# Kernel tuning notes

Measured on AMD Instinct MI355X. Metric: run time of the kernel, lower is better.

## Reference

```python
import jax, jax.numpy as jnp
import numpy as np

B, T, K = 16, 512, 128  # batch, seq_len, num_state


def setup_inputs() -> dict:
    key = jax.random.key(0)
    k1, k2, k3 = jax.random.split(key, 3)
    transition = jax.random.normal(k1, (K, K), dtype=jnp.float32)
    emission = jax.random.normal(k2, (B, T, K), dtype=jnp.float32)
    seq_lens = jax.random.randint(k3, (B,), 1, T + 1)  # lengths in [1, T]
    return {"transition": transition, "emission": emission, "seq_lens": seq_lens}


def reference(transition, emission, seq_lens):
    # potential_normalization='none' -> identity normalize().
    # combine_potentials: log phi[b, t, y_{t-1}, y_t] = trans[y_{t-1}, y_t] + emis[b, t, y_t]
    log_pot = transition[None, None, :, :] + emission[:, :, None, :]  # [B,T,K,K]

    alpha0 = emission[:, 0, :]  # [B,K]

    def step(alpha_prev, pot_t):  # alpha_prev: [B,K], pot_t: [B,K,K]
        alpha_t = jax.nn.logsumexp(alpha_prev[:, :, None] + pot_t, axis=1)
        return alpha_t, alpha_t

    # scan over time steps 1..T-1 (time-major potentials)
    _, alphas_rest = jax.lax.scan(step, alpha0, jnp.swapaxes(log_pot[:, 1:], 0, 1))
    alpha = jnp.concatenate(
        [alpha0[:, None, :], jnp.swapaxes(alphas_rest, 0, 1)], axis=1
    )  # [B,T,K]

    # gather alpha at position seq_lens - 1 per batch element
    last = jnp.take_along_axis(alpha, (seq_lens - 1)[:, None, None], axis=1)[:, 0, :]
    log_Z = jax.nn.logsumexp(last, axis=-1)  # [B]
    return alpha, log_Z
```

## Files before the change

kernel.cpp:

```cpp
#include <hip/hip_runtime.h>
#include <math.h>

#define KDIM 128
#define TLEN 512
#define BATCH 16
#define CH_L 16
#define NCH 32
#define NMAT 31

typedef _Float16 half8 __attribute__((ext_vector_type(8)));
typedef _Float16 half4 __attribute__((ext_vector_type(4)));
typedef _Float16 half2t __attribute__((ext_vector_type(2)));
typedef float floatx4 __attribute__((ext_vector_type(4)));

#if defined(__has_builtin)
#if __has_builtin(__builtin_amdgcn_fdot2)
#define HAVE_FDOT2 1
#endif
#endif

static __device__ __forceinline__ float dot2f(half2t a, half2t b, float c) {
#ifdef HAVE_FDOT2
    return __builtin_amdgcn_fdot2(a, b, c, false);
#else
    return fmaf((float)a[0], (float)b[0], fmaf((float)a[1], (float)b[1], c));
#endif
}

static __device__ __forceinline__ float dot8(const half8 v, const float4 w, float acc) {
    const uint4 r = __builtin_bit_cast(uint4, v);
    acc = dot2f(__builtin_bit_cast(half2t, w.x), __builtin_bit_cast(half2t, r.x), acc);
    acc = dot2f(__builtin_bit_cast(half2t, w.y), __builtin_bit_cast(half2t, r.y), acc);
    acc = dot2f(__builtin_bit_cast(half2t, w.z), __builtin_bit_cast(half2t, r.z), acc);
    acc = dot2f(__builtin_bit_cast(half2t, w.w), __builtin_bit_cast(half2t, r.w), acc);
    return acc;
}

static __device__ __forceinline__ void gload_lds16(const _Float16* g, _Float16* l) {
    __builtin_amdgcn_global_load_lds(
        (const __attribute__((address_space(1))) void*)g,
        (__attribute__((address_space(3))) void*)l, 16, 0, 0);
}

#define WS_PST   0
#define WS_SLOG  16252928
#define WS_AENT  16254912
#define WS_NEED  16517056


__global__ __launch_bounds__(256, 2) void crf_chunkmat4(
    const float* __restrict__ trans, const float* __restrict__ em,
    _Float16* __restrict__ Pst, float* __restrict__ Sout)
{
    const int c = blockIdx.x;
    const int b = blockIdx.y;
    const int tid = threadIdx.x;
    const int w = tid >> 6, lane = tid & 63;
    const int quad = lane >> 4, lm = lane & 15;

    __shared__ __align__(16) _Float16 buf[17408];
    __shared__ __align__(16) float gAll[16 * KDIM];
    __shared__ float mE[16];
    __shared__ float slotV[4];

    const int t0 = c * CH_L + 1;
    const float* emb = em + (size_t)b * TLEN * KDIM;

    half8 EA[2][4];
    #pragma unroll
    for (int r = 0; r < 2; ++r) {
        const int m = (2 * w + r) * 16 + lm;
        #pragma unroll
        for (int kt = 0; kt < 4; ++kt) {
            #pragma unroll
            for (int i = 0; i < 8; ++i) {
                EA[r][kt][i] = (_Float16)__expf(trans[(kt * 32 + quad * 8 + i) * KDIM + m]);
            }
        }
    }

    #pragma unroll
    for (int s = 0; s < 2; ++s) {
        int i4 = tid + s * 256;
        *(float4*)&gAll[i4 * 4] = *(const float4*)&emb[t0 * KDIM + i4 * 4];
    }
    __syncthreads();

    #pragma unroll
    for (int r2 = 0; r2 < 4; ++r2) {
        const int r = w * 4 + r2;
        float v = fmaxf(gAll[r * KDIM + lane], gAll[r * KDIM + 64 + lane]);
        #pragma unroll
        for (int o = 32; o; o >>= 1) v = fmaxf(v, __shfl_xor(v, o));
        if (lane == 0) mE[r] = v;
    }
    __syncthreads();

    #pragma unroll
    for (int s = 0; s < 8; ++s) {
        int idx = tid + s * 256;
        gAll[idx] = __expf(gAll[idx] - mE[idx >> 7]);
    }
    __syncthreads();

    for (int s = 0; s < 8; ++s) {
        int g = tid + s * 256;
        int row = g >> 4, nl = g & 15;
        int addr = row * 136 + nl * 8;
        int koct = row & 15;
        int n = (row >> 4) * 16 + nl;
        int j0 = koct * 8;
        const float* tr_ = &trans[n * KDIM + j0];
        const float* g0p = &gAll[j0];
        half8 o;
        #pragma unroll
        for (int x = 0; x < 8; ++x) o[x] = (_Float16)(__expf(tr_[x]) * g0p[x]);
        *(half8*)&buf[addr] = o;
    }
    float S = 0.f;
    if (tid == 0) {
        #pragma unroll
        for (int r = 0; r < 16; ++r) S += mE[r];
    }
    __syncthreads();

    floatx4 acc[2][8];

    for (int it = 1; it < 16; ++it) {
        #pragma unroll
        for (int r = 0; r < 2; ++r)
            #pragma unroll
            for (int nt = 0; nt < 8; ++nt)
                acc[r][nt] = (floatx4){0.f, 0.f, 0.f, 0.f};

        #pragma unroll
        for (int kt = 0; kt < 4; ++kt) {
            #pragma unroll
            for (int nt = 0; nt < 8; ++nt) {
                half8 bb = *(const half8*)&buf[(nt * 16 + kt * 4 + quad) * 136 + lm * 8];
                acc[0][nt] = __builtin_amdgcn_mfma_f32_16x16x32_f16(EA[0][kt], bb, acc[0][nt], 0, 0, 0);
                acc[1][nt] = __builtin_amdgcn_mfma_f32_16x16x32_f16(EA[1][kt], bb, acc[1][nt], 0, 0, 0);
            }
        }

        const float* gc = &gAll[it * KDIM];
        const float4 gr0 = *(const float4*)&gc[(2 * w + 0) * 16 + quad * 4];
        const float4 gr1 = *(const float4*)&gc[(2 * w + 1) * 16 + quad * 4];

        float lmax = 0.f;
        #pragma unroll
        for (int nt = 0; nt < 8; ++nt) {
            floatx4 v0 = acc[0][nt], v1 = acc[1][nt];
            float a0 = fmaxf(fmaxf(v0.x * gr0.x, v0.y * gr0.y), fmaxf(v0.z * gr0.z, v0.w * gr0.w));
            float a1 = fmaxf(fmaxf(v1.x * gr1.x, v1.y * gr1.y), fmaxf(v1.z * gr1.z, v1.w * gr1.w));
            lmax = fmaxf(lmax, fmaxf(a0, a1));
        }
        #pragma unroll
        for (int o = 32; o; o >>= 1) lmax = fmaxf(lmax, __shfl_xor(lmax, o));
        if (lane == 0) slotV[w] = lmax;
        __syncthreads();

        const float rr = fmaxf(fmaxf(slotV[0], slotV[1]), fmaxf(slotV[2], slotV[3]));
        const float rinv = 1.0f / rr;
        if (tid == 0) S += __logf(rr);

        const float4 s0 = {gr0.x * rinv, gr0.y * rinv, gr0.z * rinv, gr0.w * rinv};
        const float4 s1 = {gr1.x * rinv, gr1.y * rinv, gr1.z * rinv, gr1.w * rinv};
        const int jlb = (quad & 1) * 4;
        #pragma unroll
        for (int r = 0; r < 2; ++r) {
            const int tr = 2 * w + r;
            const int kh = tr * 2 + (quad >> 1);
            const float4 sc = r ? s1 : s0;
            #pragma unroll
            for (int nt = 0; nt < 8; ++nt) {
                const floatx4 v = acc[r][nt];
                half4 o;
                o[0] = (_Float16)(v.x * sc.x);
                o[1] = (_Float16)(v.y * sc.y);
                o[2] = (_Float16)(v.z * sc.z);
                o[3] = (_Float16)(v.w * sc.w);
                *(half4*)&buf[(nt * 16 + kh) * 136 + lm * 8 + jlb] = o;
            }
        }
        __syncthreads();
    }

    _Float16* Pc = Pst + ((size_t)(b * NMAT + c)) * 16384;
    for (int s = 0; s < 8; ++s) {
        int u = tid + s * 256;
        int l = u & 63;
        int rh = u >> 6;
        int K = rh >> 1, h = rh & 1;
        int j = 2 * l + h;
        const int base = ((K >> 1) * 16 + (j >> 3)) * 136 + (K & 1) * 64 + (j & 7);
        half8 v;
        #pragma unroll
        for (int e = 0; e < 8; ++e) v[e] = buf[base + e * 8];
        *(half8*)&Pc[u * 8] = v;
    }
    if (tid == 0) Sout[b * NMAT + c] = S;
}

__global__ __launch_bounds__(64, 1) void crf_scanw2(
    const float* __restrict__ em, const _Float16* __restrict__ Pst,
    const float* __restrict__ S, float* __restrict__ aEnter)
{
    const int b = blockIdx.x;
    const int lane = threadIdx.x;
    const int j0 = 2 * lane;

    __shared__ __align__(16) _Float16 Pbuf[2][16384];
    __shared__ __align__(16) _Float16 pbuf[KDIM];
    __shared__ float Sl[NMAT];

    const _Float16* Pb = Pst + (size_t)b * NMAT * 16384;
    float* aeb = aEnter + (size_t)b * NCH * KDIM;

    #pragma unroll
    for (int i = 0; i < 32; ++i)
        gload_lds16(Pb + i * 512 + lane * 8, &Pbuf[0][i * 512]);

    if (lane < NMAT) Sl[lane] = S[b * NMAT + lane];

    float2 a0 = *(const float2*)&em[(size_t)b * TLEN * KDIM + j0];
    float mx = fmaxf(a0.x, a0.y);
    #pragma unroll
    for (int o = 32; o; o >>= 1) mx = fmaxf(mx, __shfl_xor(mx, o));
    float L = mx;
    *(float2*)&aeb[j0] = a0;
    {
        half2t p2;
        p2[0] = (_Float16)__expf(a0.x - L);
        p2[1] = (_Float16)__expf(a0.y - L);
        ((half2t*)pbuf)[lane] = p2;
    }

    for (int c = 0; c < NMAT; ++c) {
        const int cb = c & 1, nb = cb ^ 1;

        asm volatile("s_waitcnt vmcnt(0)" ::: "memory");

        if (c + 1 < NMAT) {
            const _Float16* src = Pb + (size_t)(c + 1) * 16384;
            #pragma unroll
            for (int i = 0; i < 32; ++i)
                gload_lds16(src + i * 512 + lane * 8, &Pbuf[nb][i * 512]);
        }

        float q0 = 0.f, q1 = 0.f;
        #pragma unroll
        for (int K = 0; K < 16; ++K) {
            const float4 w = *(const float4*)&pbuf[K * 8];
            const half8 c0 = *(const half8*)&Pbuf[cb][((2 * K + 0) * 64 + lane) * 8];
            const half8 c1 = *(const half8*)&Pbuf[cb][((2 * K + 1) * 64 + lane) * 8];
            q0 = dot8(c0, w, q0);
            q1 = dot8(c1, w, q1);
        }

        const float s_c = Sl[c];
        const float sigma = __shfl(q0, 0);
        const float base = L + s_c;
        float2 st;
        st.x = base + __logf(q0);
        st.y = base + __logf(q1);
        *(float2*)&aeb[(c + 1) * KDIM + j0] = st;
        const float ri = 1.0f / sigma;
        half2t p2;
        p2[0] = (_Float16)(q0 * ri);
        p2[1] = (_Float16)(q1 * ri);
        ((half2t*)pbuf)[lane] = p2;
        L = base + __logf(sigma);
    }
}

__global__ __launch_bounds__(64, 1) void crf_replayw(
    const float* __restrict__ trans, const float* __restrict__ em,
    const int* __restrict__ seq_lens, const float* __restrict__ aEnter,
    float* __restrict__ alpha, float* __restrict__ logZ)
{
    const int c = blockIdx.x, b = blockIdx.y;
    const int l = threadIdx.x;

    __shared__ __align__(16) _Float16 pbuf[KDIM];

    half2t Ea[64], Eb[64];
    #pragma unroll
    for (int t2 = 0; t2 < 64; ++t2) {
        const float* r0 = &trans[(2 * t2) * KDIM];
        const float* r1 = &trans[(2 * t2 + 1) * KDIM];
        half2t ea, eb;
        ea[0] = (_Float16)__expf(r0[l]);
        ea[1] = (_Float16)__expf(r1[l]);
        eb[0] = (_Float16)__expf(r0[l + 64]);
        eb[1] = (_Float16)__expf(r1[l + 64]);
        Ea[t2] = ea;
        Eb[t2] = eb;
    }

    const int len = seq_lens[b];
    const float* emb = em + (size_t)b * TLEN * KDIM;
    float* outb = alpha + (size_t)b * TLEN * KDIM;
    const float* ae = aEnter + ((size_t)b * NCH + c) * KDIM;

    float a0 = ae[l], a1 = ae[l + 64];
    if (c == 0) {
        a0 = emb[l];
        a1 = emb[l + 64];
    }
    float mx = fmaxf(a0, a1);
    #pragma unroll
    for (int o = 32; o; o >>= 1) mx = fmaxf(mx, __shfl_xor(mx, o));
    float L = mx;
    pbuf[l]      = (_Float16)__expf(a0 - L);
    pbuf[l + 64] = (_Float16)__expf(a1 - L);

    float la0 = 0.f, la1 = -INFINITY;
    if (c == 0) {
        outb[l] = a0;
        outb[l + 64] = a1;
        if (len == 1) { la0 = a0; la1 = a1; }
    }

    const int t_begin = c * CH_L + 1;
    const int t_end = (c == NCH - 1) ? (TLEN - 1) : (c * CH_L + CH_L);

    float e0 = emb[t_begin * KDIM + l];
    float e1 = emb[t_begin * KDIM + l + 64];

    for (int t = t_begin; t <= t_end; ++t) {
        float n0 = 0.f, n1 = 0.f;
        if (t < t_end) {
            n0 = emb[(t + 1) * KDIM + l];
            n1 = emb[(t + 1) * KDIM + l + 64];
        }

        float q0 = 0.f, q1 = 0.f;
        #pragma unroll
        for (int s = 0; s < 16; ++s) {
            const float4 w = *(const float4*)&pbuf[s * 8];
            const half2t p0 = __builtin_bit_cast(half2t, w.x);
            const half2t p1 = __builtin_bit_cast(half2t, w.y);
            const half2t p2 = __builtin_bit_cast(half2t, w.z);
            const half2t p3 = __builtin_bit_cast(half2t, w.w);
            q0 = dot2f(p0, Ea[4 * s + 0], q0);
            q0 = dot2f(p1, Ea[4 * s + 1], q0);
            q0 = dot2f(p2, Ea[4 * s + 2], q0);
            q0 = dot2f(p3, Ea[4 * s + 3], q0);
            q1 = dot2f(p0, Eb[4 * s + 0], q1);
            q1 = dot2f(p1, Eb[4 * s + 1], q1);
            q1 = dot2f(p2, Eb[4 * s + 2], q1);
            q1 = dot2f(p3, Eb[4 * s + 3], q1);
        }

        const float A0 = e0 + L + __logf(q0);
        const float A1 = e1 + L + __logf(q1);
        outb[t * KDIM + l] = A0;
        outb[t * KDIM + l + 64] = A1;
        if (t == len - 1) { la0 = A0; la1 = A1; }

        const float sigma = __shfl(q0, 0);
        const float ri = 1.0f / sigma;
        pbuf[l]      = (_Float16)(q0 * ri * __expf(e0));
        pbuf[l + 64] = (_Float16)(q1 * ri * __expf(e1));
        L += __logf(sigma);
        e0 = n0; e1 = n1;
    }

    const bool blockowns = (len == 1) ? (c == 0) : (((len - 2) >> 4) == c);
    if (blockowns) {
        float m2 = fmaxf(la0, la1);
        #pragma unroll
        for (int o = 32; o; o >>= 1) m2 = fmaxf(m2, __shfl_xor(m2, o));
        float e = __expf(la0 - m2) + __expf(la1 - m2);
        #pragma unroll
        for (int o = 32; o; o >>= 1) e += __shfl_xor(e, o);
        if (l == 0) logZ[b] = m2 + __logf(e);
    }
}

__global__ __launch_bounds__(256) void crf_forward_fallback(
    const float* __restrict__ trans, const float* __restrict__ em,
    const int* __restrict__ seq_lens, float* __restrict__ alpha_out,
    float* __restrict__ logZ_out)
{
    const int b = blockIdx.x;
    const int tid = threadIdx.x;
    const int j = tid & (KDIM - 1);
    const int h = tid >> 7;

    __shared__ __align__(16) float p_lds[KDIM];
    __shared__ float part[KDIM];
    __shared__ float red[8];

    float Ereg[64];
    #pragma unroll
    for (int k = 0; k < 64; ++k) Ereg[k] = __expf(trans[(h * 64 + k) * KDIM + j]);

    const int len = seq_lens[b];
    const float* emb = em + (size_t)b * TLEN * KDIM;
    float* outb = alpha_out + (size_t)b * TLEN * KDIM;

    float a = 0.f, last_a = 0.f;
    if (h == 0) {
        a = emb[j];
        outb[j] = a;
        if (len == 1) last_a = a;
    }
    for (int t = 1; t < TLEN; ++t) {
        {
            float v = (h == 0) ? a : -INFINITY;
            #pragma unroll
            for (int o = 32; o >= 1; o >>= 1) v = fmaxf(v, __shfl_xor(v, o));
            if ((tid & 63) == 0) red[tid >> 6] = v;
        }
        __syncthreads();
        const float m = fmaxf(red[0], red[1]);
        if (h == 0) p_lds[j] = __expf(a - m);
        __syncthreads();
        float em_t = 0.f;
        if (h == 0) em_t = emb[t * KDIM + j];
        float acc0 = 0.f, acc1 = 0.f, acc2 = 0.f, acc3 = 0.f;
        const float4* p4 = (const float4*)(p_lds + h * 64);
        #pragma unroll
        for (int k4 = 0; k4 < 16; ++k4) {
            float4 pv = p4[k4];
            acc0 = fmaf(pv.x, Ereg[4 * k4 + 0], acc0);
            acc1 = fmaf(pv.y, Ereg[4 * k4 + 1], acc1);
            acc2 = fmaf(pv.z, Ereg[4 * k4 + 2], acc2);
            acc3 = fmaf(pv.w, Ereg[4 * k4 + 3], acc3);
        }
        const float acc = (acc0 + acc1) + (acc2 + acc3);
        if (h == 1) part[j] = acc;
        __syncthreads();
        if (h == 0) {
            const float q = acc + part[j];
            a = em_t + m + __logf(q);
            outb[t * KDIM + j] = a;
            if (t == len - 1) last_a = a;
        }
    }
    {
        float v = (h == 0) ? last_a : -INFINITY;
        #pragma unroll
        for (int o = 32; o >= 1; o >>= 1) v = fmaxf(v, __shfl_xor(v, o));
        if ((tid & 63) == 0) red[tid >> 6] = v;
    }
    __syncthreads();
    const float m2 = fmaxf(red[0], red[1]);
    float e = (h == 0) ? __expf(last_a - m2) : 0.f;
    #pragma unroll
    for (int o = 32; o >= 1; o >>= 1) e += __shfl_xor(e, o);
    if ((tid & 63) == 0) red[4 + (tid >> 6)] = e;
    __syncthreads();
    if (tid == 0) logZ_out[b] = m2 + logf(red[4] + red[5]);
}

extern "C" void kernel_launch(void* const* d_in, const int* in_sizes, int n_in,
                              void* d_out, int out_size, void* d_ws, size_t ws_size,
                              hipStream_t stream) {
    const float* trans    = (const float*)d_in[0];
    const float* em       = (const float*)d_in[1];
    const int*   seq_lens = (const int*)d_in[2];

    float* alpha_out = (float*)d_out;
    float* logZ_out  = alpha_out + (size_t)BATCH * TLEN * KDIM;

    if (ws_size < (size_t)WS_NEED) {
        crf_forward_fallback<<<BATCH, 256, 0, stream>>>(trans, em, seq_lens,
                                                        alpha_out, logZ_out);
        return;
    }

    char* ws = (char*)d_ws;
    _Float16* Pst  = (_Float16*)(ws + WS_PST);
    float*    Slog = (float*)(ws + WS_SLOG);
    float*    aEnt = (float*)(ws + WS_AENT);

    crf_chunkmat4<<<dim3(NMAT, BATCH), 256, 0, stream>>>(trans, em, Pst, Slog);
    crf_scanw2<<<BATCH, 64, 0, stream>>>(em, Pst, Slog, aEnt);
    crf_replayw<<<dim3(NCH, BATCH), 64, 0, stream>>>(trans, em, seq_lens, aEnt,
                                                     alpha_out, logZ_out);
}
```

Measured before the change: 166.1 us.

## Use per-column scaled chunk matrix products with vector scale for CRF scan

```diff
diff --git a/kernel.cpp b/kernel.cpp
--- a/kernel.cpp
+++ b/kernel.cpp
@@ -42,11 +42,269 @@
         (__attribute__((address_space(3))) void*)l, 16, 0, 0);
 }
 
-#define WS_PST   0
-#define WS_SLOG  16252928
-#define WS_AENT  16254912
-#define WS_NEED  16517056
-
+#define WSN_PST   0
+#define WSN_SVEC  16252928
+#define WSN_AENT  16506880
+#define WSN_NEED  16769024
+#define WSO_PST   0
+#define WSO_SLOG  16252928
+#define WSO_AENT  16254912
+#define WSO_NEED  16517056
+
+__global__ __launch_bounds__(256, 2) void crf_chunkcols(
+    const float* __restrict__ trans, const float* __restrict__ em,
+    _Float16* __restrict__ Pst, float* __restrict__ Svec)
+{
+    const int c = blockIdx.x;
+    const int b = blockIdx.y;
+    const int tid = threadIdx.x;
+    const int w = tid >> 6, lane = tid & 63;
+    const int quad = lane >> 4, lm = lane & 15;
+
+    __shared__ __align__(16) _Float16 Flds[128 * 136];
+    __shared__ __align__(16) _Float16 Wscr[4][4608];
+    __shared__ __align__(16) float gAll[16 * KDIM];
+
+    const int t0 = c * CH_L + 1;
+    const float* emb = em + (size_t)b * TLEN * KDIM;
+
+    {
+        const int m = tid & 127, kh = tid >> 7;
+        #pragma unroll
+        for (int kk = 0; kk < 8; ++kk) {
+            const int k0 = kh * 64 + kk * 8;
+            half8 o;
+            #pragma unroll
+            for (int j = 0; j < 8; ++j)
+                o[j] = (_Float16)__expf(trans[(k0 + j) * KDIM + m]);
+            *(half8*)&Flds[m * 136 + k0] = o;
+        }
+    }
+    {
+        const int i8 = tid * 8;
+        const float4 e0 = *(const float4*)&emb[t0 * KDIM + i8];
+        const float4 e1 = *(const float4*)&emb[t0 * KDIM + i8 + 4];
+        float4 g0, g1;
+        g0.x = __expf(e0.x); g0.y = __expf(e0.y); g0.z = __expf(e0.z); g0.w = __expf(e0.w);
+        g1.x = __expf(e1.x); g1.y = __expf(e1.y); g1.z = __expf(e1.z); g1.w = __expf(e1.w);
+        *(float4*)&gAll[i8] = g0;
+        *(float4*)&gAll[i8 + 4] = g1;
+    }
+    __syncthreads();
+
+    _Float16* Wb = Wscr[w];
+    float sc0, sc1;
+    half8 Bf[4][2];
+
+    {
+        float tv[4][2][8];
+        float cm0 = 0.f, cm1 = 0.f;
+        #pragma unroll
+        for (int kt = 0; kt < 4; ++kt) {
+            const int r0 = kt * 32 + quad * 8;
+            const float4 ga = *(const float4*)&gAll[r0];
+            const float4 gb = *(const float4*)&gAll[r0 + 4];
+            const float gg[8] = {ga.x, ga.y, ga.z, ga.w, gb.x, gb.y, gb.z, gb.w};
+            #pragma unroll
+            for (int nt = 0; nt < 2; ++nt) {
+                const int n = 32 * w + nt * 16 + lm;
+                const float4 ta = *(const float4*)&trans[(size_t)n * KDIM + r0];
+                const float4 tb = *(const float4*)&trans[(size_t)n * KDIM + r0 + 4];
+                const float tt[8] = {ta.x, ta.y, ta.z, ta.w, tb.x, tb.y, tb.z, tb.w};
+                float mx = 0.f;
+                #pragma unroll
+                for (int j = 0; j < 8; ++j) {
+                    const float v = __expf(tt[j]) * gg[j];
+                    tv[kt][nt][j] = v;
+                    mx = fmaxf(mx, v);
+                }
+                if (nt == 0) cm0 = fmaxf(cm0, mx); else cm1 = fmaxf(cm1, mx);
+            }
+        }
+        cm0 = fmaxf(cm0, __shfl_xor(cm0, 16));
+        cm0 = fmaxf(cm0, __shfl_xor(cm0, 32));
+        cm1 = fmaxf(cm1, __shfl_xor(cm1, 16));
+        cm1 = fmaxf(cm1, __shfl_xor(cm1, 32));
+        const float ri0 = 1.0f / cm0, ri1 = 1.0f / cm1;
+        sc0 = __logf(cm0);
+        sc1 = __logf(cm1);
+        #pragma unroll
+        for (int kt = 0; kt < 4; ++kt)
+            #pragma unroll
+            for (int nt = 0; nt < 2; ++nt) {
+                const float ri = nt ? ri1 : ri0;
+                #pragma unroll
+                for (int j = 0; j < 8; ++j)
+                    Bf[kt][nt][j] = (_Float16)(tv[kt][nt][j] * ri);
+            }
+    }
+
+    const floatx4 z4 = {0.f, 0.f, 0.f, 0.f};
+    for (int it = 1; it < 16; ++it) {
+        floatx4 acc[8][2];
+        #pragma unroll
+        for (int mt = 0; mt < 8; ++mt) {
+            const half8 Af = *(const half8*)&Flds[lm * 136 + quad * 8 + mt * 2176];
+            acc[mt][0] = __builtin_amdgcn_mfma_f32_16x16x32_f16(Af, Bf[0][0], z4, 0, 0, 0);
+            acc[mt][1] = __builtin_amdgcn_mfma_f32_16x16x32_f16(Af, Bf[0][1], z4, 0, 0, 0);
+        }
+        #pragma unroll
+        for (int kt = 1; kt < 4; ++kt) {
+            #pragma unroll
+            for (int mt = 0; mt < 8; ++mt) {
+                const half8 Af = *(const half8*)&Flds[lm * 136 + quad * 8 + mt * 2176 + kt * 32];
+                acc[mt][0] = __builtin_amdgcn_mfma_f32_16x16x32_f16(Af, Bf[kt][0], acc[mt][0], 0, 0, 0);
+                acc[mt][1] = __builtin_amdgcn_mfma_f32_16x16x32_f16(Af, Bf[kt][1], acc[mt][1], 0, 0, 0);
+            }
+        }
+        const float* g = &gAll[it * KDIM];
+        float cm0 = 0.f, cm1 = 0.f;
+        #pragma unroll
+        for (int mt = 0; mt < 8; ++mt) {
+            const float4 gv = *(const float4*)&g[mt * 16 + quad * 4];
+            floatx4 v0 = acc[mt][0], v1 = acc[mt][1];
+            v0.x *= gv.x; v0.y *= gv.y; v0.z *= gv.z; v0.w *= gv.w;
+            v1.x *= gv.x; v1.y *= gv.y; v1.z *= gv.z; v1.w *= gv.w;
+            acc[mt][0] = v0; acc[mt][1] = v1;
+            cm0 = fmaxf(cm0, fmaxf(fmaxf(v0.x, v0.y), fmaxf(v0.z, v0.w)));
+            cm1 = fmaxf(cm1, fmaxf(fmaxf(v1.x, v1.y), fmaxf(v1.z, v1.w)));
+        }
+        cm0 = fmaxf(cm0, __shfl_xor(cm0, 16));
+        cm0 = fmaxf(cm0, __shfl_xor(cm0, 32));
+        cm1 = fmaxf(cm1, __shfl_xor(cm1, 16));
+        cm1 = fmaxf(cm1, __shfl_xor(cm1, 32));
+        const float ri0 = 1.0f / cm0, ri1 = 1.0f / cm1;
+        sc0 += __logf(cm0);
+        sc1 += __logf(cm1);
+
+        if (it < 15) {
+            #pragma unroll
+            for (int mt = 0; mt < 8; ++mt)
+                #pragma unroll
+                for (int nt = 0; nt < 2; ++nt) {
+                    const floatx4 v = acc[mt][nt];
+                    const float ri = nt ? ri1 : ri0;
+                    half4 o;
+                    o[0] = (_Float16)(v.x * ri);
+                    o[1] = (_Float16)(v.y * ri);
+                    o[2] = (_Float16)(v.z * ri);
+                    o[3] = (_Float16)(v.w * ri);
+                    *(half4*)&Wb[lm * 136 + quad * 4 + nt * 2176 + mt * 16] = o;
+                }
+            asm volatile("s_waitcnt lgkmcnt(0)" ::: "memory");
+            #pragma unroll
+            for (int kt = 0; kt < 4; ++kt)
+                #pragma unroll
+                for (int nt = 0; nt < 2; ++nt)
+                    Bf[kt][nt] = *(const half8*)&Wb[lm * 136 + quad * 8 + nt * 2176 + kt * 32];
+        } else {
+            #pragma unroll
+            for (int mt = 0; mt < 8; ++mt)
+                #pragma unroll
+                for (int nt = 0; nt < 2; ++nt) {
+                    const floatx4 v = acc[mt][nt];
+                    const float ri = nt ? ri1 : ri0;
+                    const int ba = quad * 144 + lm + mt * 576 + nt * 16;
+                    Wb[ba]       = (_Float16)(v.x * ri);
+                    Wb[ba + 36]  = (_Float16)(v.y * ri);
+                    Wb[ba + 72]  = (_Float16)(v.z * ri);
+                    Wb[ba + 108] = (_Float16)(v.w * ri);
+                }
+            asm volatile("s_waitcnt lgkmcnt(0)" ::: "memory");
+        }
+    }
+
+    _Float16* Pc = Pst + ((size_t)(b * NMAT + c)) * 16384;
+    #pragma unroll
+    for (int Kl = 0; Kl < 4; ++Kl)
+        #pragma unroll
+        for (int h = 0; h < 2; ++h) {
+            const half4 lo = *(const half4*)&Wb[(2 * lane + h) * 36 + Kl * 8];
+            const half4 hi = *(const half4*)&Wb[(2 * lane + h) * 36 + Kl * 8 + 4];
+            half8 v;
+            #pragma unroll
+            for (int e = 0; e < 4; ++e) { v[e] = lo[e]; v[4 + e] = hi[e]; }
+            const int u = (2 * (4 * w + Kl) + h) * 64 + lane;
+            *(half8*)&Pc[(size_t)u * 8] = v;
+        }
+    if (quad == 0) {
+        float* sp = Svec + ((size_t)(b * NMAT + c)) * KDIM + 32 * w;
+        sp[lm] = sc0;
+        sp[lm + 16] = sc1;
+    }
+}
+
+__global__ __launch_bounds__(64, 1) void crf_scanw3(
+    const float* __restrict__ em, const _Float16* __restrict__ Pst,
+    const float* __restrict__ Svec, float* __restrict__ aEnter)
+{
+    const int b = blockIdx.x;
+    const int lane = threadIdx.x;
+    const int j0 = 2 * lane;
+
+    __shared__ __align__(16) _Float16 Pbuf[2][16384];
+    __shared__ __align__(16) _Float16 pbuf[KDIM];
+
+    const _Float16* Pb = Pst + (size_t)b * NMAT * 16384;
+    const float* svb = Svec + (size_t)b * NMAT * KDIM;
+    float* aeb = aEnter + (size_t)b * NCH * KDIM;
+
+    #pragma unroll
+    for (int i = 0; i < 32; ++i)
+        gload_lds16(Pb + i * 512 + lane * 8, &Pbuf[0][i * 512]);
+
+    float2 a0 = *(const float2*)&em[(size_t)b * TLEN * KDIM + j0];
+    float mx = fmaxf(a0.x, a0.y);
+    #pragma unroll
+    for (int o = 32; o; o >>= 1) mx = fmaxf(mx, __shfl_xor(mx, o));
+    *(float2*)&aeb[j0] = a0;
+    float lq0 = a0.x - mx, lq1 = a0.y - mx;
+    float L = mx;
+    float2 sv = *(const float2*)&svb[j0];
+
+    for (int c = 0; c < NMAT; ++c) {
+        const int cb = c & 1, nb = cb ^ 1;
+
+        asm volatile("s_waitcnt vmcnt(0)" ::: "memory");
+
+        if (c + 1 < NMAT) {
+            const _Float16* src = Pb + (size_t)(c + 1) * 16384;
+            #pragma unroll
+            for (int i = 0; i < 32; ++i)
+                gload_lds16(src + i * 512 + lane * 8, &Pbuf[nb][i * 512]);
+        }
+
+        const float v0 = lq0 + sv.x, v1 = lq1 + sv.y;
+        float M = fmaxf(v0, v1);
+        #pragma unroll
+        for (int o = 32; o; o >>= 1) M = fmaxf(M, __shfl_xor(M, o));
+        half2t p2;
+        p2[0] = (_Float16)__expf(v0 - M);
+        p2[1] = (_Float16)__expf(v1 - M);
+        ((half2t*)pbuf)[lane] = p2;
+        if (c + 1 < NMAT) sv = *(const float2*)&svb[(size_t)(c + 1) * KDIM + j0];
+
+        float q0 = 0.f, q1 = 0.f;
+        #pragma unroll
+        for (int K = 0; K < 16; ++K) {
+            const float4 wv = *(const float4*)&pbuf[K * 8];
+            const half8 c0 = *(const half8*)&Pbuf[cb][((2 * K + 0) * 64 + lane) * 8];
+            const half8 c1 = *(const half8*)&Pbuf[cb][((2 * K + 1) * 64 + lane) * 8];
+            q0 = dot8(c0, wv, q0);
+            q1 = dot8(c1, wv, q1);
+        }
+
+        const float base = L + M;
+        const float lg0 = __logf(q0), lg1 = __logf(q1);
+        float2 st;
+        st.x = base + lg0;
+        st.y = base + lg1;
+        *(float2*)&aeb[(size_t)(c + 1) * KDIM + j0] = st;
+        lq0 = lg0;
+        lq1 = lg1;
+        L = base;
+    }
+}
 
 __global__ __launch_bounds__(256, 2) void crf_chunkmat4(
     const float* __restrict__ trans, const float* __restrict__ em,
@@ -466,19 +724,26 @@
     float* alpha_out = (float*)d_out;
     float* logZ_out  = alpha_out + (size_t)BATCH * TLEN * KDIM;
 
-    if (ws_size < (size_t)WS_NEED) {
+    char* ws = (char*)d_ws;
+
+    if (ws_size >= (size_t)WSN_NEED) {
+        _Float16* Pst  = (_Float16*)(ws + WSN_PST);
+        float*    Svec = (float*)(ws + WSN_SVEC);
+        float*    aEnt = (float*)(ws + WSN_AENT);
+        crf_chunkcols<<<dim3(NMAT, BATCH), 256, 0, stream>>>(trans, em, Pst, Svec);
+        crf_scanw3<<<BATCH, 64, 0, stream>>>(em, Pst, Svec, aEnt);
+        crf_replayw<<<dim3(NCH, BATCH), 64, 0, stream>>>(trans, em, seq_lens, aEnt,
+                                                         alpha_out, logZ_out);
+    } else if (ws_size >= (size_t)WSO_NEED) {
+        _Float16* Pst  = (_Float16*)(ws + WSO_PST);
+        float*    Slog = (float*)(ws + WSO_SLOG);
+        float*    aEnt = (float*)(ws + WSO_AENT);
+        crf_chunkmat4<<<dim3(NMAT, BATCH), 256, 0, stream>>>(trans, em, Pst, Slog);
+        crf_scanw2<<<BATCH, 64, 0, stream>>>(em, Pst, Slog, aEnt);
+        crf_replayw<<<dim3(NCH, BATCH), 64, 0, stream>>>(trans, em, seq_lens, aEnt,
+                                                         alpha_out, logZ_out);
+    } else {
         crf_forward_fallback<<<BATCH, 256, 0, stream>>>(trans, em, seq_lens,
                                                         alpha_out, logZ_out);
-        return;
-    }
-
-    char* ws = (char*)d_ws;
-    _Float16* Pst  = (_Float16*)(ws + WS_PST);
-    float*    Slog = (float*)(ws + WS_SLOG);
-    float*    aEnt = (float*)(ws + WS_AENT);
-
-    crf_chunkmat4<<<dim3(NMAT, BATCH), 256, 0, stream>>>(trans, em, Pst, Slog);
-    crf_scanw2<<<BATCH, 64, 0, stream>>>(em, Pst, Slog, aEnt);
-    crf_replayw<<<dim3(NCH, BATCH), 64, 0, stream>>>(trans, em, seq_lens, aEnt,
-                                                     alpha_out, logZ_out);
-}
+    }
+}
```

New measurement: 157.9 us. -4.9%, faster.

## Use per-column scaling in chunk matrices and triple-buffer the scan prefetch

Applied to the files above, without the earlier changes.

```diff
diff --git a/kernel.cpp b/kernel.cpp
--- a/kernel.cpp
+++ b/kernel.cpp
@@ -42,15 +42,14 @@
         (__attribute__((address_space(3))) void*)l, 16, 0, 0);
 }
 
-#define WS_PST   0
-#define WS_SLOG  16252928
-#define WS_AENT  16254912
-#define WS_NEED  16517056
-
-
-__global__ __launch_bounds__(256, 2) void crf_chunkmat4(
+#define WSN_PST   0
+#define WSN_SVEC  16252928
+#define WSN_AENT  16506880
+#define WSN_NEED  16769024
+
+__global__ __launch_bounds__(256, 2) void crf_chunkcols2(
     const float* __restrict__ trans, const float* __restrict__ em,
-    _Float16* __restrict__ Pst, float* __restrict__ Sout)
+    _Float16* __restrict__ Pst, float* __restrict__ Svec)
 {
     const int c = blockIdx.x;
     const int b = blockIdx.y;
@@ -58,219 +57,240 @@
     const int w = tid >> 6, lane = tid & 63;
     const int quad = lane >> 4, lm = lane & 15;
 
-    __shared__ __align__(16) _Float16 buf[17408];
+    __shared__ __align__(16) _Float16 Flds[128 * 136];
+    __shared__ __align__(16) _Float16 Wscr[4][4608];
     __shared__ __align__(16) float gAll[16 * KDIM];
-    __shared__ float mE[16];
-    __shared__ float slotV[4];
 
     const int t0 = c * CH_L + 1;
     const float* emb = em + (size_t)b * TLEN * KDIM;
 
-    half8 EA[2][4];
-    #pragma unroll
-    for (int r = 0; r < 2; ++r) {
-        const int m = (2 * w + r) * 16 + lm;
+    {
+        const int m = tid & 127, kh = tid >> 7;
+        #pragma unroll
+        for (int kk = 0; kk < 8; ++kk) {
+            const int k0 = kh * 64 + kk * 8;
+            half8 o;
+            #pragma unroll
+            for (int j = 0; j < 8; ++j)
+                o[j] = (_Float16)__expf(trans[(k0 + j) * KDIM + m]);
+            *(half8*)&Flds[m * 136 + k0] = o;
+        }
+    }
+    {
+        const int i8 = tid * 8;
+        const float4 e0 = *(const float4*)&emb[t0 * KDIM + i8];
+        const float4 e1 = *(const float4*)&emb[t0 * KDIM + i8 + 4];
+        float4 g0, g1;
+        g0.x = __expf(e0.x); g0.y = __expf(e0.y); g0.z = __expf(e0.z); g0.w = __expf(e0.w);
+        g1.x = __expf(e1.x); g1.y = __expf(e1.y); g1.z = __expf(e1.z); g1.w = __expf(e1.w);
+        *(float4*)&gAll[i8] = g0;
+        *(float4*)&gAll[i8 + 4] = g1;
+    }
+    __syncthreads();
+
+    _Float16* Wb = Wscr[w];
+    float sc[2];
+    half8 Bf[4][2];
+
+    #pragma unroll
+    for (int nt = 0; nt < 2; ++nt) {
+        float tv[4][8];
+        float cm = 0.f;
+        const int n = 32 * w + nt * 16 + lm;
         #pragma unroll
         for (int kt = 0; kt < 4; ++kt) {
-            #pragma unroll
-            for (int i = 0; i < 8; ++i) {
-                EA[r][kt][i] = (_Float16)__expf(trans[(kt * 32 + quad * 8 + i) * KDIM + m]);
+            const int r0 = kt * 32 + quad * 8;
+            const float4 ga = *(const float4*)&gAll[r0];
+            const float4 gb = *(const float4*)&gAll[r0 + 4];
+            const float gg[8] = {ga.x, ga.y, ga.z, ga.w, gb.x, gb.y, gb.z, gb.w};
+            const float4 ta = *(const float4*)&trans[(size_t)n * KDIM + r0];
+            const float4 tb = *(const float4*)&trans[(size_t)n * KDIM + r0 + 4];
+            const float tt[8] = {ta.x, ta.y, ta.z, ta.w, tb.x, tb.y, tb.z, tb.w};
+            #pragma unroll
+            for (int j = 0; j < 8; ++j) {
+                const float v = __expf(tt[j]) * gg[j];
+                tv[kt][j] = v;
+                cm = fmaxf(cm, v);
             }
         }
-    }
-
-    #pragma unroll
-    for (int s = 0; s < 2; ++s) {
-        int i4 = tid + s * 256;
-        *(float4*)&gAll[i4 * 4] = *(const float4*)&emb[t0 * KDIM + i4 * 4];
-    }
-    __syncthreads();
-
-    #pragma unroll
-    for (int r2 = 0; r2 < 4; ++r2) {
-        const int r = w * 4 + r2;
-        float v = fmaxf(gAll[r * KDIM + lane], gAll[r * KDIM + 64 + lane]);
-        #pragma unroll
-        for (int o = 32; o; o >>= 1) v = fmaxf(v, __shfl_xor(v, o));
-        if (lane == 0) mE[r] = v;
-    }
-    __syncthreads();
-
-    #pragma unroll
-    for (int s = 0; s < 8; ++s) {
-        int idx = tid + s * 256;
-        gAll[idx] = __expf(gAll[idx] - mE[idx >> 7]);
-    }
-    __syncthreads();
-
-    for (int s = 0; s < 8; ++s) {
-        int g = tid + s * 256;
-        int row = g >> 4, nl = g & 15;
-        int addr = row * 136 + nl * 8;
-        int koct = row & 15;
-        int n = (row >> 4) * 16 + nl;
-        int j0 = koct * 8;
-        const float* tr_ = &trans[n * KDIM + j0];
-        const float* g0p = &gAll[j0];
-        half8 o;
-        #pragma unroll
-        for (int x = 0; x < 8; ++x) o[x] = (_Float16)(__expf(tr_[x]) * g0p[x]);
-        *(half8*)&buf[addr] = o;
-    }
-    float S = 0.f;
-    if (tid == 0) {
-        #pragma unroll
-        for (int r = 0; r < 16; ++r) S += mE[r];
-    }
-    __syncthreads();
-
-    floatx4 acc[2][8];
-
+        cm = fmaxf(cm, __shfl_xor(cm, 16));
+        cm = fmaxf(cm, __shfl_xor(cm, 32));
+        const float ri = 1.0f / cm;
+        sc[nt] = __logf(cm);
+        #pragma unroll
+        for (int kt = 0; kt < 4; ++kt)
+            #pragma unroll
+            for (int j = 0; j < 8; ++j)
+                Bf[kt][nt][j] = (_Float16)(tv[kt][j] * ri);
+    }
+
+    half8 Af[8][4];
+    #pragma unroll
+    for (int mt = 0; mt < 8; ++mt)
+        #pragma unroll
+        for (int kt = 0; kt < 4; ++kt)
+            Af[mt][kt] = *(const half8*)&Flds[lm * 136 + quad * 8 + mt * 2176 + kt * 32];
+
+    const floatx4 z4 = {0.f, 0.f, 0.f, 0.f};
     for (int it = 1; it < 16; ++it) {
         #pragma unroll
-        for (int r = 0; r < 2; ++r)
-            #pragma unroll
-            for (int nt = 0; nt < 8; ++nt)
-                acc[r][nt] = (floatx4){0.f, 0.f, 0.f, 0.f};
-
-        #pragma unroll
-        for (int kt = 0; kt < 4; ++kt) {
-            #pragma unroll
-            for (int nt = 0; nt < 8; ++nt) {
-                half8 bb = *(const half8*)&buf[(nt * 16 + kt * 4 + quad) * 136 + lm * 8];
-                acc[0][nt] = __builtin_amdgcn_mfma_f32_16x16x32_f16(EA[0][kt], bb, acc[0][nt], 0, 0, 0);
-                acc[1][nt] = __builtin_amdgcn_mfma_f32_16x16x32_f16(EA[1][kt], bb, acc[1][nt], 0, 0, 0);
+        for (int nt = 0; nt < 2; ++nt) {
+            floatx4 acc[8];
+            #pragma unroll
+            for (int mt = 0; mt < 8; ++mt)
+                acc[mt] = __builtin_amdgcn_mfma_f32_16x16x32_f16(Af[mt][0], Bf[0][nt], z4, 0, 0, 0);
+            #pragma unroll
+            for (int kt = 1; kt < 4; ++kt)
+                #pragma unroll
+                for (int mt = 0; mt < 8; ++mt)
+                    acc[mt] = __builtin_amdgcn_mfma_f32_16x16x32_f16(Af[mt][kt], Bf[kt][nt], acc[mt], 0, 0, 0);
+
+            const float* g = &gAll[it * KDIM];
+            float cm = 0.f;
+            #pragma unroll
+            for (int mt = 0; mt < 8; ++mt) {
+                const float4 gv = *(const float4*)&g[mt * 16 + quad * 4];
+                floatx4 v = acc[mt];
+                v.x *= gv.x; v.y *= gv.y; v.z *= gv.z; v.w *= gv.w;
+                acc[mt] = v;
+                cm = fmaxf(cm, fmaxf(fmaxf(v.x, v.y), fmaxf(v.z, v.w)));
             }
-        }
-
-        const float* gc = &gAll[it * KDIM];
-        const float4 gr0 = *(const float4*)&gc[(2 * w + 0) * 16 + quad * 4];
-        const float4 gr1 = *(const float4*)&gc[(2 * w + 1) * 16 + quad * 4];
-
-        float lmax = 0.f;
-        #pragma unroll
-        for (int nt = 0; nt < 8; ++nt) {
-            floatx4 v0 = acc[0][nt], v1 = acc[1][nt];
-            float a0 = fmaxf(fmaxf(v0.x * gr0.x, v0.y * gr0.y), fmaxf(v0.z * gr0.z, v0.w * gr0.w));
-            float a1 = fmaxf(fmaxf(v1.x * gr1.x, v1.y * gr1.y), fmaxf(v1.z * gr1.z, v1.w * gr1.w));
-            lmax = fmaxf(lmax, fmaxf(a0, a1));
-        }
-        #pragma unroll
-        for (int o = 32; o; o >>= 1) lmax = fmaxf(lmax, __shfl_xor(lmax, o));
-        if (lane == 0) slotV[w] = lmax;
-        __syncthreads();
-
-        const float rr = fmaxf(fmaxf(slotV[0], slotV[1]), fmaxf(slotV[2], slotV[3]));
-        const float rinv = 1.0f / rr;
-        if (tid == 0) S += __logf(rr);
-
-        const float4 s0 = {gr0.x * rinv, gr0.y * rinv, gr0.z * rinv, gr0.w * rinv};
-        const float4 s1 = {gr1.x * rinv, gr1.y * rinv, gr1.z * rinv, gr1.w * rinv};
-        const int jlb = (quad & 1) * 4;
-        #pragma unroll
-        for (int r = 0; r < 2; ++r) {
-            const int tr = 2 * w + r;
-            const int kh = tr * 2 + (quad >> 1);
-            const float4 sc = r ? s1 : s0;
-            #pragma unroll
-            for (int nt = 0; nt < 8; ++nt) {
-                const floatx4 v = acc[r][nt];
-                half4 o;
-                o[0] = (_Float16)(v.x * sc.x);
-                o[1] = (_Float16)(v.y * sc.y);
-                o[2] = (_Float16)(v.z * sc.z);
-                o[3] = (_Float16)(v.w * sc.w);
-                *(half4*)&buf[(nt * 16 + kh) * 136 + lm * 8 + jlb] = o;
+            cm = fmaxf(cm, __shfl_xor(cm, 16));
+            cm = fmaxf(cm, __shfl_xor(cm, 32));
+            const float ri = 1.0f / cm;
+            sc[nt] += __logf(cm);
+
+            if (it < 15) {
+                #pragma unroll
+                for (int mt = 0; mt < 8; ++mt) {
+                    const floatx4 v = acc[mt];
+                    half4 o;
+                    o[0] = (_Float16)(v.x * ri);
+                    o[1] = (_Float16)(v.y * ri);
+                    o[2] = (_Float16)(v.z * ri);
+                    o[3] = (_Float16)(v.w * ri);
+                    *(half4*)&Wb[lm * 136 + quad * 4 + nt * 2176 + mt * 16] = o;
+                }
+            } else {
+                #pragma unroll
+                for (int mt = 0; mt < 8; ++mt) {
+                    const floatx4 v = acc[mt];
+                    const int ba = quad * 144 + lm + mt * 576 + nt * 16;
+                    Wb[ba]       = (_Float16)(v.x * ri);
+                    Wb[ba + 36]  = (_Float16)(v.y * ri);
+                    Wb[ba + 72]  = (_Float16)(v.z * ri);
+                    Wb[ba + 108] = (_Float16)(v.w * ri);
+                }
             }
         }
-        __syncthreads();
+        asm volatile("s_waitcnt lgkmcnt(0)" ::: "memory");
+        if (it < 15) {
+            #pragma unroll
+            for (int kt = 0; kt < 4; ++kt)
+                #pragma unroll
+                for (int nt = 0; nt < 2; ++nt)
+                    Bf[kt][nt] = *(const half8*)&Wb[lm * 136 + quad * 8 + nt * 2176 + kt * 32];
+        }
     }
 
     _Float16* Pc = Pst + ((size_t)(b * NMAT + c)) * 16384;
-    for (int s = 0; s < 8; ++s) {
-        int u = tid + s * 256;
-        int l = u & 63;
-        int rh = u >> 6;
-        int K = rh >> 1, h = rh & 1;
-        int j = 2 * l + h;
-        const int base = ((K >> 1) * 16 + (j >> 3)) * 136 + (K & 1) * 64 + (j & 7);
-        half8 v;
-        #pragma unroll
-        for (int e = 0; e < 8; ++e) v[e] = buf[base + e * 8];
-        *(half8*)&Pc[u * 8] = v;
-    }
-    if (tid == 0) Sout[b * NMAT + c] = S;
-}
-
-__global__ __launch_bounds__(64, 1) void crf_scanw2(
+    #pragma unroll
+    for (int Kl = 0; Kl < 4; ++Kl)
+        #pragma unroll
+        for (int h = 0; h < 2; ++h) {
+            const half4 lo = *(const half4*)&Wb[(2 * lane + h) * 36 + Kl * 8];
+            const half4 hi = *(const half4*)&Wb[(2 * lane + h) * 36 + Kl * 8 + 4];
+            half8 v;
+            #pragma unroll
+            for (int e = 0; e < 4; ++e) { v[e] = lo[e]; v[4 + e] = hi[e]; }
+            const int u = (2 * (4 * w + Kl) + h) * 64 + lane;
+            *(half8*)&Pc[(size_t)u * 8] = v;
+        }
+    if (quad == 0) {
+        float* sp = Svec + ((size_t)(b * NMAT + c)) * KDIM + 32 * w;
+        sp[lm] = sc[0];
+        sp[lm + 16] = sc[1];
+    }
+}
+
+__global__ __launch_bounds__(64, 1) void crf_scanw4(
     const float* __restrict__ em, const _Float16* __restrict__ Pst,
-    const float* __restrict__ S, float* __restrict__ aEnter)
+    const float* __restrict__ Svec, float* __restrict__ aEnter)
 {
     const int b = blockIdx.x;
     const int lane = threadIdx.x;
     const int j0 = 2 * lane;
 
-    __shared__ __align__(16) _Float16 Pbuf[2][16384];
+    __shared__ __align__(16) _Float16 Pbuf[3][16384];
     __shared__ __align__(16) _Float16 pbuf[KDIM];
-    __shared__ float Sl[NMAT];
 
     const _Float16* Pb = Pst + (size_t)b * NMAT * 16384;
+    const float* svb = Svec + (size_t)b * NMAT * KDIM;
     float* aeb = aEnter + (size_t)b * NCH * KDIM;
 
     #pragma unroll
     for (int i = 0; i < 32; ++i)
         gload_lds16(Pb + i * 512 + lane * 8, &Pbuf[0][i * 512]);
-
-    if (lane < NMAT) Sl[lane] = S[b * NMAT + lane];
+    #pragma unroll
+    for (int i = 0; i < 32; ++i)
+        gload_lds16(Pb + 16384 + i * 512 + lane * 8, &Pbuf[1][i * 512]);
 
     float2 a0 = *(const float2*)&em[(size_t)b * TLEN * KDIM + j0];
     float mx = fmaxf(a0.x, a0.y);
     #pragma unroll
     for (int o = 32; o; o >>= 1) mx = fmaxf(mx, __shfl_xor(mx, o));
+    *(float2*)&aeb[j0] = a0;
+    float lq0 = a0.x - mx, lq1 = a0.y - mx;
     float L = mx;
-    *(float2*)&aeb[j0] = a0;
-    {
+    float2 sv = *(const float2*)&svb[j0];
+
+    int cb = 0;
+    for (int c = 0; c < NMAT; ++c) {
+        if (c + 1 < NMAT) {
+            asm volatile("s_waitcnt vmcnt(32)" ::: "memory");
+        } else {
+            asm volatile("s_waitcnt vmcnt(0)" ::: "memory");
+        }
+
+        if (c + 2 < NMAT) {
+            const _Float16* src = Pb + (size_t)(c + 2) * 16384;
+            _Float16* dst = &Pbuf[(cb + 2) % 3][0];
+            #pragma unroll
+            for (int i = 0; i < 32; ++i)
+                gload_lds16(src + i * 512 + lane * 8, &dst[i * 512]);
+        }
+
+        const float v0 = lq0 + sv.x, v1 = lq1 + sv.y;
+        float M = fmaxf(v0, v1);
+        #pragma unroll
+        for (int o = 32; o; o >>= 1) M = fmaxf(M, __shfl_xor(M, o));
         half2t p2;
-        p2[0] = (_Float16)__expf(a0.x - L);
-        p2[1] = (_Float16)__expf(a0.y - L);
+        p2[0] = (_Float16)__expf(v0 - M);
+        p2[1] = (_Float16)__expf(v1 - M);
         ((half2t*)pbuf)[lane] = p2;
-    }
-
-    for (int c = 0; c < NMAT; ++c) {
-        const int cb = c & 1, nb = cb ^ 1;
-
-        asm volatile("s_waitcnt vmcnt(0)" ::: "memory");
-
-        if (c + 1 < NMAT) {
-            const _Float16* src = Pb + (size_t)(c + 1) * 16384;
-            #pragma unroll
-            for (int i = 0; i < 32; ++i)
-                gload_lds16(src + i * 512 + lane * 8, &Pbuf[nb][i * 512]);
-        }
-
+        if (c + 1 < NMAT) sv = *(const float2*)&svb[(size_t)(c + 1) * KDIM + j0];
+
+        const _Float16* Pcur = &Pbuf[cb][0];
         float q0 = 0.f, q1 = 0.f;
         #pragma unroll
         for (int K = 0; K < 16; ++K) {
-            const float4 w = *(const float4*)&pbuf[K * 8];
-            const half8 c0 = *(const half8*)&Pbuf[cb][((2 * K + 0) * 64 + lane) * 8];
-            const half8 c1 = *(const half8*)&Pbuf[cb][((2 * K + 1) * 64 + lane) * 8];
-            q0 = dot8(c0, w, q0);
-            q1 = dot8(c1, w, q1);
-        }
-
-        const float s_c = Sl[c];
-        const float sigma = __shfl(q0, 0);
-        const float base = L + s_c;
+            const float4 wv = *(const float4*)&pbuf[K * 8];
+            const half8 c0 = *(const half8*)&Pcur[((2 * K + 0) * 64 + lane) * 8];
+            const half8 c1 = *(const half8*)&Pcur[((2 * K + 1) * 64 + lane) * 8];
+            q0 = dot8(c0, wv, q0);
+            q1 = dot8(c1, wv, q1);
+        }
+
+        const float base = L + M;
+        const float lg0 = __logf(q0), lg1 = __logf(q1);
         float2 st;
-        st.x = base + __logf(q0);
-        st.y = base + __logf(q1);
-        *(float2*)&aeb[(c + 1) * KDIM + j0] = st;
-        const float ri = 1.0f / sigma;
-        half2t p2;
-        p2[0] = (_Float16)(q0 * ri);
-        p2[1] = (_Float16)(q1 * ri);
-        ((half2t*)pbuf)[lane] = p2;
-        L = base + __logf(sigma);
+        st.x = base + lg0;
+        st.y = base + lg1;
+        *(float2*)&aeb[(size_t)(c + 1) * KDIM + j0] = st;
+        lq0 = lg0;
+        lq1 = lg1;
+        L = base;
+        cb = (cb + 1) % 3;
     }
 }
 
@@ -466,19 +486,18 @@
     float* alpha_out = (float*)d_out;
     float* logZ_out  = alpha_out + (size_t)BATCH * TLEN * KDIM;
 
-    if (ws_size < (size_t)WS_NEED) {
+    char* ws = (char*)d_ws;
+
+    if (ws_size >= (size_t)WSN_NEED) {
+        _Float16* Pst  = (_Float16*)(ws + WSN_PST);
+        float*    Svec = (float*)(ws + WSN_SVEC);
+        float*    aEnt = (float*)(ws + WSN_AENT);
+        crf_chunkcols2<<<dim3(NMAT, BATCH), 256, 0, stream>>>(trans, em, Pst, Svec);
+        crf_scanw4<<<BATCH, 64, 0, stream>>>(em, Pst, Svec, aEnt);
+        crf_replayw<<<dim3(NCH, BATCH), 64, 0, stream>>>(trans, em, seq_lens, aEnt,
+                                                         alpha_out, logZ_out);
+    } else {
         crf_forward_fallback<<<BATCH, 256, 0, stream>>>(trans, em, seq_lens,
                                                         alpha_out, logZ_out);
-        return;
-    }
-
-    char* ws = (char*)d_ws;
-    _Float16* Pst  = (_Float16*)(ws + WS_PST);
-    float*    Slog = (float*)(ws + WS_SLOG);
-    float*    aEnt = (float*)(ws + WS_AENT);
-
-    crf_chunkmat4<<<dim3(NMAT, BATCH), 256, 0, stream>>>(trans, em, Pst, Slog);
-    crf_scanw2<<<BATCH, 64, 0, stream>>>(em, Pst, Slog, aEnt);
-    crf_replayw<<<dim3(NCH, BATCH), 64, 0, stream>>>(trans, em, seq_lens, aEnt,
-                                                     alpha_out, logZ_out);
-}
+    }
+}
```

Result: faster. 156.4 us (-5.8%).
